# Kernel optimization log

Hardware: AMD Instinct MI355X
Metric: run time of the kernel (lower is better)

## Reference

```python
import jax, jax.numpy as jnp
import numpy as np

N = 50000   # residue nodes
E = 800000  # edges per edge type
T = 3       # edge types
L = 3       # conv layers (len(hidden_channels)-1)
IN, H, ENC, OUT, K = 64, 128, 100, 32, 128
COMMIT = 0.25
EPS = 1e-5


def gelu(x):
    return jax.nn.gelu(x, approximate=False)  # torch nn.GELU default (erf)


def setup_inputs() -> dict:
    key = jax.random.key(0)
    ks = iter(jax.random.split(key, 40))
    p = lambda shp, s=0.05: jax.random.normal(next(ks), shp, jnp.float32) * s
    inp = {
        'x_res': p((N, IN), 1.0),
        'x_AA': p((N, 20), 1.0),
        'edge_index': jax.random.randint(next(ks), (T, 2, E), 0, N, jnp.int32),
        # input block
        'ln_gamma': jnp.ones((IN,), jnp.float32),
        'ln_beta': jnp.zeros((IN,), jnp.float32),
        'W1': p((IN, 2 * H)), 'b1': jnp.zeros((2 * H,), jnp.float32),
        'W2': p((2 * H, H)), 'b2': jnp.zeros((H,), jnp.float32),
        # body: SAGE convs, [layer, edge_type, ...]
        'sage_Wl': p((L, T, H, H)),  # applied to aggregated neighbors
        'sage_Wr': p((L, T, H, H)),  # applied to root
        'sage_b': jnp.zeros((L, T, H), jnp.float32),
        # GraphNorm per layer
        'gn_weight': jnp.ones((L, H), jnp.float32),
        'gn_bias': jnp.zeros((L, H), jnp.float32),
        'gn_scale': jnp.ones((L, H), jnp.float32),  # mean_scale
        # head
        'Wh1': p((H * L, ENC)), 'bh1': jnp.zeros((ENC,), jnp.float32),
        'Wh2': p((ENC, ENC)), 'bh2': jnp.zeros((ENC,), jnp.float32),
        'Wo1': p((ENC + 20, ENC)), 'bo1': jnp.zeros((ENC,), jnp.float32),
        'Wo2': p((ENC, ENC)), 'bo2': jnp.zeros((ENC,), jnp.float32),
        'Wo3': p((ENC, OUT)), 'bo3': jnp.zeros((OUT,), jnp.float32),
        # VQ codebook
        'codebook': p((K, OUT), 0.5),
    }
    return inp


def _sage(x, src, dst, Wl, Wr, b):
    # SAGEConv, mean aggregation: out = Wl @ mean_{src->dst}(x[src]) + Wr @ x + b
    msg = x[src]                                             # [E, H] gather
    s = jax.ops.segment_sum(msg, dst, num_segments=N)        # [N, H] scatter-add
    cnt = jax.ops.segment_sum(jnp.ones((msg.shape[0],), x.dtype), dst, num_segments=N)
    agg = s / jnp.maximum(cnt, 1.0)[:, None]
    return agg @ Wl + x @ Wr + b


def _graphnorm(x, weight, bias, scale):
    # PyG GraphNorm over a single graph
    out = x - scale * x.mean(0)
    var = (out * out).mean(0)
    return out * jax.lax.rsqrt(var + EPS) * weight + bias


def reference(x_res, x_AA, edge_index, ln_gamma, ln_beta, W1, b1, W2, b2,
              sage_Wl, sage_Wr, sage_b, gn_weight, gn_bias, gn_scale,
              Wh1, bh1, Wh2, bh2, Wo1, bo1, Wo2, bo2, Wo3, bo3, codebook):
    # input: LayerNorm + (dropout = identity in eval) + inmlp
    mu = x_res.mean(-1, keepdims=True)
    var = x_res.var(-1, keepdims=True)
    xr = (x_res - mu) * jax.lax.rsqrt(var + EPS) * ln_gamma + ln_beta
    x = gelu(gelu(xr @ W1 + b1) @ W2 + b2)                   # [N, H]

    # body: per-edge-type SAGE conv -> stack-mean -> GELU -> GraphNorm; JK cat
    x_save = []
    for i in range(L):
        xs = [_sage(x, edge_index[t, 0], edge_index[t, 1],
                    sage_Wl[i, t], sage_Wr[i, t], sage_b[i, t]) for t in range(T)]
        x = jnp.mean(jnp.stack(xs, 0), 0)
        x = gelu(x)
        x = _graphnorm(x, gn_weight[i], gn_bias[i], gn_scale[i])
        x_save.append(x)
    x = jnp.concatenate(x_save, axis=1)                      # [N, H*L] JumpingKnowledge cat

    # head
    x = gelu(gelu(x @ Wh1 + bh1) @ Wh2 + bh2)
    x = jnp.concatenate([x, x_AA], axis=1)
    x = gelu(x @ Wo1 + bo1)
    x = gelu(x @ Wo2 + bo2)
    x = jnp.tanh(x @ Wo3 + bo3)                              # [N, OUT]

    # VectorQuantizer (straight-through)
    d = (jnp.sum(x * x, 1, keepdims=True)
         - 2.0 * x @ codebook.T
         + jnp.sum(codebook * codebook, 1)[None, :])         # [N, K]
    idx = jnp.argmin(d, axis=1)
    q = codebook[idx]                                        # [N, OUT]
    e_latent = jnp.mean((jax.lax.stop_gradient(q) - x) ** 2)
    q_latent = jnp.mean((q - jax.lax.stop_gradient(x)) ** 2)
    vq_loss = q_latent + COMMIT * e_latent
    z_q = x + jax.lax.stop_gradient(q - x)
    return z_q, vq_loss
```

## Files before the change

kernel.cpp:

```cpp
#include <hip/hip_runtime.h>

#define N_ 50000
#define E_ 800000
#define T_ 3
#define NG_ (T_ * N_)
#define EPS_ 1e-5f

__device__ __forceinline__ float gelu_f(float x) {
    return 0.5f * x * (1.0f + erff(x * 0.70710678118654752440f));
}

__global__ void k_prep(const float* __restrict__ Wl, const float* __restrict__ Wr,
                       const float* __restrict__ b, float* wls, float* wra, float* ba) {
    int i = blockIdx.x * 256 + threadIdx.x;
    const float third = 1.0f / 3.0f;
    if (i < 9 * 128 * 128) wls[i] = Wl[i] * third;
    if (i < 3 * 128 * 128) {
        int l = i >> 14, rem = i & 16383;
        const float* p = Wr + l * 3 * 16384 + rem;
        wra[i] = (p[0] + p[16384] + p[32768]) * third;
    }
    if (i < 3 * 128) {
        int l = i >> 7, c = i & 127;
        const float* p = b + l * 3 * 128 + c;
        ba[i] = (p[0] + p[128] + p[256]) * third;
    }
}

__global__ void k_count(const int* __restrict__ EI, int* cnt) {
    int i = blockIdx.x * 256 + threadIdx.x;
    if (i >= T_ * E_) return;
    int t = i / E_, e = i - t * E_;
    int d = EI[(t * 2 + 1) * E_ + e];
    atomicAdd(&cnt[t * N_ + d], 1);
}

__global__ void k_alloc(const int* __restrict__ cnt, int* __restrict__ cursor,
                        int* __restrict__ rpA, int* __restrict__ rpB, float* __restrict__ inv) {
    int i = blockIdx.x * 256 + threadIdx.x;
    if (i >= NG_) return;
    int c = cnt[i];
    inv[i] = 1.0f / (float)(c > 0 ? c : 1);
    int s = atomicAdd(cursor, c);
    rpA[i] = s;
    rpB[i] = s;
}

__global__ void k_place(const int* __restrict__ EI, int* __restrict__ rpB, int* __restrict__ csr) {
    int i = blockIdx.x * 256 + threadIdx.x;
    if (i >= T_ * E_) return;
    int t = i / E_, e = i - t * E_;
    int s = EI[(t * 2) * E_ + e];
    int d = EI[(t * 2 + 1) * E_ + e];
    int pos = atomicAdd(&rpB[t * N_ + d], 1);
    csr[pos] = s;
}

__global__ __launch_bounds__(256) void k_inmlp(
    const float* __restrict__ xres, const float* __restrict__ gam, const float* __restrict__ bet,
    const float* __restrict__ W1, const float* __restrict__ b1,
    const float* __restrict__ W2, const float* __restrict__ b2, float* __restrict__ x0) {
    __shared__ float xr[32][68];
    __shared__ float h1[32][260];
    int tid = threadIdx.x;
    int base = blockIdx.x * 32;
    for (int i = 0; i < 2; ++i) {
        int f4 = i * 256 + tid;
        int r = f4 >> 4, c4 = f4 & 15;
        float4 v = make_float4(0.f, 0.f, 0.f, 0.f);
        int gr = base + r;
        if (gr < N_) v = *(const float4*)&xres[gr * 64 + c4 * 4];
        *(float4*)&xr[r][c4 * 4] = v;
    }
    __syncthreads();
    if (tid < 32) {
        int r = tid;
        float s = 0.f;
        for (int k = 0; k < 64; ++k) s += xr[r][k];
        float mu = s * (1.0f / 64.0f);
        float v = 0.f;
        for (int k = 0; k < 64; ++k) { float d = xr[r][k] - mu; v += d * d; }
        float rs = rsqrtf(v * (1.0f / 64.0f) + EPS_);
        for (int k = 0; k < 64; ++k)
            xr[r][k] = (xr[r][k] - mu) * rs * gam[k] + bet[k];
    }
    __syncthreads();
    {
        int tx = tid & 63, ty = tid >> 6;
        int c0 = tx * 4, r0 = ty * 8;
        float acc[8][4];
        for (int r = 0; r < 8; ++r)
            for (int j = 0; j < 4; ++j) acc[r][j] = b1[c0 + j];
        for (int k0 = 0; k0 < 64; k0 += 4) {
            float4 a[8], w[4];
            for (int r = 0; r < 8; ++r) a[r] = *(const float4*)&xr[r0 + r][k0];
            for (int kk = 0; kk < 4; ++kk) w[kk] = *(const float4*)&W1[(k0 + kk) * 256 + c0];
            for (int kk = 0; kk < 4; ++kk)
                for (int r = 0; r < 8; ++r) {
                    float as = (&a[r].x)[kk];
                    acc[r][0] = fmaf(as, w[kk].x, acc[r][0]);
                    acc[r][1] = fmaf(as, w[kk].y, acc[r][1]);
                    acc[r][2] = fmaf(as, w[kk].z, acc[r][2]);
                    acc[r][3] = fmaf(as, w[kk].w, acc[r][3]);
                }
        }
        for (int r = 0; r < 8; ++r)
            for (int j = 0; j < 4; ++j) h1[r0 + r][c0 + j] = gelu_f(acc[r][j]);
    }
    __syncthreads();
    {
        int tx = tid & 31, ty = tid >> 5;
        int c0 = tx * 4, r0 = ty * 4;
        float acc[4][4];
        for (int r = 0; r < 4; ++r)
            for (int j = 0; j < 4; ++j) acc[r][j] = b2[c0 + j];
        for (int k0 = 0; k0 < 256; k0 += 4) {
            float4 a[4], w[4];
            for (int r = 0; r < 4; ++r) a[r] = *(const float4*)&h1[r0 + r][k0];
            for (int kk = 0; kk < 4; ++kk) w[kk] = *(const float4*)&W2[(k0 + kk) * 128 + c0];
            for (int kk = 0; kk < 4; ++kk)
                for (int r = 0; r < 4; ++r) {
                    float as = (&a[r].x)[kk];
                    acc[r][0] = fmaf(as, w[kk].x, acc[r][0]);
                    acc[r][1] = fmaf(as, w[kk].y, acc[r][1]);
                    acc[r][2] = fmaf(as, w[kk].z, acc[r][2]);
                    acc[r][3] = fmaf(as, w[kk].w, acc[r][3]);
                }
        }
        for (int r = 0; r < 4; ++r) {
            int gr = base + r0 + r;
            if (gr < N_) {
                float4 v = make_float4(gelu_f(acc[r][0]), gelu_f(acc[r][1]),
                                       gelu_f(acc[r][2]), gelu_f(acc[r][3]));
                *(float4*)&x0[(long)gr * 128 + c0] = v;
            }
        }
    }
}

__global__ __launch_bounds__(256) void k_gather(
    const int* __restrict__ rpA, const int* __restrict__ cnt, const int* __restrict__ csr,
    const float* __restrict__ inv, const float* __restrict__ X, int ldx, float* __restrict__ agg) {
    int tid = threadIdx.x;
    int g = blockIdx.x * 4 + (tid >> 6);
    if (g >= NG_) return;
    int lane = tid & 63;
    int half = lane >> 5;
    int f = (lane & 31) * 4;
    int start = rpA[g];
    int end = start + cnt[g];
    float4 s = make_float4(0.f, 0.f, 0.f, 0.f);
    for (int e = start + half; e < end; e += 2) {
        int sn = csr[e];
        const float4 v = *(const float4*)&X[(long)sn * ldx + f];
        s.x += v.x; s.y += v.y; s.z += v.z; s.w += v.w;
    }
    s.x += __shfl_xor(s.x, 32);
    s.y += __shfl_xor(s.y, 32);
    s.z += __shfl_xor(s.z, 32);
    s.w += __shfl_xor(s.w, 32);
    if (half == 0) {
        float iv = inv[g];
        float4 o = make_float4(s.x * iv, s.y * iv, s.z * iv, s.w * iv);
        *(float4*)&agg[(long)g * 128 + f] = o;
    }
}

__global__ __launch_bounds__(256) void k_gemm_body(
    const float* __restrict__ X, int ldx, const float* __restrict__ agg,
    const float* __restrict__ wls_l, const float* __restrict__ wra_l, const float* __restrict__ ba_l,
    float* __restrict__ g_out, float* __restrict__ cs_l) {
    __shared__ float xs[64][132];
    __shared__ float sd[8][128];
    int tid = threadIdx.x;
    int base = blockIdx.x * 64;
    int tx = tid & 31, ty = tid >> 5;
    int c0 = tx * 4, r0 = ty * 8;
    float acc[8][4];
    for (int r = 0; r < 8; ++r)
        for (int j = 0; j < 4; ++j) acc[r][j] = ba_l[c0 + j];
    for (int seg = 0; seg < 4; ++seg) {
        const float* src; long ld;
        if (seg < 3) { src = agg + ((long)seg * N_ + base) * 128; ld = 128; }
        else         { src = X + (long)base * ldx; ld = ldx; }
        __syncthreads();
        for (int i = 0; i < 8; ++i) {
            int f4 = i * 256 + tid;
            int r = f4 >> 5, c4 = f4 & 31;
            float4 v = make_float4(0.f, 0.f, 0.f, 0.f);
            if (base + r < N_) v = *(const float4*)&src[(long)r * ld + c4 * 4];
            *(float4*)&xs[r][c4 * 4] = v;
        }
        __syncthreads();
        const float* W = (seg < 3) ? (wls_l + seg * 16384) : wra_l;
        for (int k0 = 0; k0 < 128; k0 += 4) {
            float4 a[8], w[4];
            for (int r = 0; r < 8; ++r) a[r] = *(const float4*)&xs[r0 + r][k0];
            for (int kk = 0; kk < 4; ++kk) w[kk] = *(const float4*)&W[(k0 + kk) * 128 + c0];
            for (int kk = 0; kk < 4; ++kk)
                for (int r = 0; r < 8; ++r) {
                    float as = (&a[r].x)[kk];
                    acc[r][0] = fmaf(as, w[kk].x, acc[r][0]);
                    acc[r][1] = fmaf(as, w[kk].y, acc[r][1]);
                    acc[r][2] = fmaf(as, w[kk].z, acc[r][2]);
                    acc[r][3] = fmaf(as, w[kk].w, acc[r][3]);
                }
        }
    }
    float csum[4] = {0.f, 0.f, 0.f, 0.f};
    for (int r = 0; r < 8; ++r) {
        int gr = base + r0 + r;
        if (gr < N_) {
            float g0 = gelu_f(acc[r][0]), g1 = gelu_f(acc[r][1]);
            float g2 = gelu_f(acc[r][2]), g3 = gelu_f(acc[r][3]);
            *(float4*)&g_out[(long)gr * 128 + c0] = make_float4(g0, g1, g2, g3);
            csum[0] += g0; csum[1] += g1; csum[2] += g2; csum[3] += g3;
        }
    }
    *(float4*)&sd[ty][c0] = make_float4(csum[0], csum[1], csum[2], csum[3]);
    __syncthreads();
    if (tid < 128) {
        float t = 0.f;
        for (int i = 0; i < 8; ++i) t += sd[i][tid];
        atomicAdd(&cs_l[tid], t);
    }
}

__global__ __launch_bounds__(256) void k_pass2(const float* __restrict__ g,
                                               const float* __restrict__ cs_l,
                                               const float* __restrict__ gsc, float* __restrict__ cq_l) {
    __shared__ float sd[256];
    int tid = threadIdx.x;
    int c = tid & 127, half = tid >> 7;
    int base = blockIdx.x * 128 + half * 64;
    float sm = gsc[c] * (cs_l[c] / 50000.0f);
    float s = 0.f;
    for (int i = 0; i < 64; ++i) {
        int r = base + i;
        if (r < N_) { float o = g[(long)r * 128 + c] - sm; s += o * o; }
    }
    sd[tid] = s;
    __syncthreads();
    if (tid < 128) atomicAdd(&cq_l[c], sd[tid] + sd[tid + 128]);
}
__global__ __launch_bounds__(256) void k_pass3(const float* __restrict__ g,
                                               const float* __restrict__ cs_l, const float* __restrict__ cq_l,
                                               const float* __restrict__ gsc,
                                               const float* __restrict__ gw, const float* __restrict__ gb,
                                               float* __restrict__ xs_l) {
    int tid = threadIdx.x;
    int c = tid & 127, half = tid >> 7;
    int base = blockIdx.x * 128 + half * 64;
    float sm = gsc[c] * (cs_l[c] / 50000.0f);
    float var = cq_l[c] / 50000.0f;
    float mul = rsqrtf(var + EPS_) * gw[c];
    float add = gb[c];
    for (int i = 0; i < 64; ++i) {
        int r = base + i;
        if (r < N_) xs_l[(long)r * 384 + c] = (g[(long)r * 128 + c] - sm) * mul + add;
    }
}

__global__ __launch_bounds__(256) void k_head1(const float* __restrict__ xsave,
    const float* __restrict__ Wh1, const float* __restrict__ bh1,
    const float* __restrict__ Wh2, const float* __restrict__ bh2,
    float* __restrict__ h2out) {
    __shared__ float at[64][68];
    __shared__ float h1b[64][104];
    int tid = threadIdx.x;
    int base = blockIdx.x * 64;
    int tx = tid & 31, ty = tid >> 5;
    int c0 = tx * 4, r0 = ty * 8;
    bool valid = (c0 < 100);
    float acc[8][4];
    for (int r = 0; r < 8; ++r)
        for (int j = 0; j < 4; ++j) acc[r][j] = valid ? bh1[c0 + j] : 0.f;
    for (int kt = 0; kt < 6; ++kt) {
        __syncthreads();
        for (int i = 0; i < 4; ++i) {
            int f4 = i * 256 + tid;
            int r = f4 >> 4, c4 = f4 & 15;
            float4 v = make_float4(0.f, 0.f, 0.f, 0.f);
            int gr = base + r;
            if (gr < N_) v = *(const float4*)&xsave[(long)gr * 384 + kt * 64 + c4 * 4];
            *(float4*)&at[r][c4 * 4] = v;
        }
        __syncthreads();
        if (valid) {
            for (int k0 = 0; k0 < 64; k0 += 4) {
                float4 a[8], w[4];
                for (int r = 0; r < 8; ++r) a[r] = *(const float4*)&at[r0 + r][k0];
                for (int kk = 0; kk < 4; ++kk) w[kk] = *(const float4*)&Wh1[(kt * 64 + k0 + kk) * 100 + c0];
                for (int kk = 0; kk < 4; ++kk)
                    for (int r = 0; r < 8; ++r) {
                        float as = (&a[r].x)[kk];
                        acc[r][0] = fmaf(as, w[kk].x, acc[r][0]);
                        acc[r][1] = fmaf(as, w[kk].y, acc[r][1]);
                        acc[r][2] = fmaf(as, w[kk].z, acc[r][2]);
                        acc[r][3] = fmaf(as, w[kk].w, acc[r][3]);
                    }
            }
        }
    }
    __syncthreads();
    if (valid)
        for (int r = 0; r < 8; ++r)
            for (int j = 0; j < 4; ++j) h1b[r0 + r][c0 + j] = gelu_f(acc[r][j]);
    __syncthreads();
    {
        float acc2[8][4];
        for (int r = 0; r < 8; ++r)
            for (int j = 0; j < 4; ++j) acc2[r][j] = valid ? bh2[c0 + j] : 0.f;
        if (valid) {
            for (int k0 = 0; k0 < 100; k0 += 4) {
                float4 a[8], w[4];
                for (int r = 0; r < 8; ++r) a[r] = *(const float4*)&h1b[r0 + r][k0];
                for (int kk = 0; kk < 4; ++kk) w[kk] = *(const float4*)&Wh2[(k0 + kk) * 100 + c0];
                for (int kk = 0; kk < 4; ++kk)
                    for (int r = 0; r < 8; ++r) {
                        float as = (&a[r].x)[kk];
                        acc2[r][0] = fmaf(as, w[kk].x, acc2[r][0]);
                        acc2[r][1] = fmaf(as, w[kk].y, acc2[r][1]);
                        acc2[r][2] = fmaf(as, w[kk].z, acc2[r][2]);
                        acc2[r][3] = fmaf(as, w[kk].w, acc2[r][3]);
                    }
            }
            for (int r = 0; r < 8; ++r) {
                int gr = base + r0 + r;
                if (gr < N_) {
                    float4 v = make_float4(gelu_f(acc2[r][0]), gelu_f(acc2[r][1]),
                                           gelu_f(acc2[r][2]), gelu_f(acc2[r][3]));
                    *(float4*)&h2out[(long)gr * 100 + c0] = v;
                }
            }
        }
    }
}

__global__ __launch_bounds__(128) void k_head2(const float* __restrict__ h2,
    const float* __restrict__ xAA,
    const float* __restrict__ Wo1, const float* __restrict__ bo1,
    const float* __restrict__ Wo2, const float* __restrict__ bo2,
    const float* __restrict__ Wo3, const float* __restrict__ bo3,
    const float* __restrict__ cb, float* __restrict__ zq, float* __restrict__ loss) {
    __shared__ __align__(16) float smem[13216];
    float* A  = smem;
    float* B  = smem + 3968;
    float* XF = smem + 7296;
    float* CB = smem + 8448;
    float* CC = smem + 13056;
    float* SR = smem + 13184;
    int tid = threadIdx.x;
    int base = blockIdx.x * 32;
    for (int i = 0; i < 8; ++i) {
        int f4 = i * 128 + tid;
        int k = f4 >> 3, j4 = f4 & 7;
        float4 v = *(const float4*)&cb[k * 32 + j4 * 4];
        *(float4*)&CB[k * 36 + j4 * 4] = v;
    }
    for (int i = 0; i < 7; ++i) {
        int f4 = i * 128 + tid;
        if (f4 < 800) {
            int r = f4 / 25, c4 = f4 - r * 25;
            float4 v = make_float4(0.f, 0.f, 0.f, 0.f);
            int gr = base + r;
            if (gr < N_) v = *(const float4*)&h2[(long)gr * 100 + c4 * 4];
            *(float4*)&A[r * 124 + c4 * 4] = v;
        }
    }
    for (int i = 0; i < 2; ++i) {
        int f4 = i * 128 + tid;
        if (f4 < 160) {
            int r = f4 / 5, c4 = f4 - r * 5;
            float4 v = make_float4(0.f, 0.f, 0.f, 0.f);
            int gr = base + r;
            if (gr < N_) v = *(const float4*)&xAA[(long)gr * 20 + c4 * 4];
            *(float4*)&A[r * 124 + 100 + c4 * 4] = v;
        }
    }
    __syncthreads();
    if (tid < 128) {
        float s = 0.f;
        for (int j = 0; j < 32; ++j) { float v = CB[tid * 36 + j]; s += v * v; }
        CC[tid] = s;
    }
    int tx = tid & 31, ty = tid >> 5;
    int c0 = tx * 4, r0 = ty * 8;
    bool valid = (c0 < 100);
    {
        float acc[8][4];
        for (int r = 0; r < 8; ++r)
            for (int j = 0; j < 4; ++j) acc[r][j] = valid ? bo1[c0 + j] : 0.f;
        if (valid) {
            for (int k0 = 0; k0 < 120; k0 += 4) {
                float4 a[8], w[4];
                for (int r = 0; r < 8; ++r) a[r] = *(const float4*)&A[(r0 + r) * 124 + k0];
                for (int kk = 0; kk < 4; ++kk) w[kk] = *(const float4*)&Wo1[(k0 + kk) * 100 + c0];
                for (int kk = 0; kk < 4; ++kk)
                    for (int r = 0; r < 8; ++r) {
                        float as = (&a[r].x)[kk];
                        acc[r][0] = fmaf(as, w[kk].x, acc[r][0]);
                        acc[r][1] = fmaf(as, w[kk].y, acc[r][1]);
                        acc[r][2] = fmaf(as, w[kk].z, acc[r][2]);
                        acc[r][3] = fmaf(as, w[kk].w, acc[r][3]);
                    }
            }
        }
        __syncthreads();
        if (valid)
            for (int r = 0; r < 8; ++r)
                for (int j = 0; j < 4; ++j) B[(r0 + r) * 104 + c0 + j] = gelu_f(acc[r][j]);
    }
    __syncthreads();
    {
        float acc[8][4];
        for (int r = 0; r < 8; ++r)
            for (int j = 0; j < 4; ++j) acc[r][j] = valid ? bo2[c0 + j] : 0.f;
        if (valid) {
            for (int k0 = 0; k0 < 100; k0 += 4) {
                float4 a[8], w[4];
                for (int r = 0; r < 8; ++r) a[r] = *(const float4*)&B[(r0 + r) * 104 + k0];
                for (int kk = 0; kk < 4; ++kk) w[kk] = *(const float4*)&Wo2[(k0 + kk) * 100 + c0];
                for (int kk = 0; kk < 4; ++kk)
                    for (int r = 0; r < 8; ++r) {
                        float as = (&a[r].x)[kk];
                        acc[r][0] = fmaf(as, w[kk].x, acc[r][0]);
                        acc[r][1] = fmaf(as, w[kk].y, acc[r][1]);
                        acc[r][2] = fmaf(as, w[kk].z, acc[r][2]);
                        acc[r][3] = fmaf(as, w[kk].w, acc[r][3]);
                    }
            }
        }
        __syncthreads();
        if (valid)
            for (int r = 0; r < 8; ++r)
                for (int j = 0; j < 4; ++j) A[(r0 + r) * 124 + c0 + j] = gelu_f(acc[r][j]);
    }
    __syncthreads();
    {
        int c0b = (tid & 7) * 4, rg = tid >> 3;
        int r0b = rg * 2;
        float acc[2][4];
        for (int r = 0; r < 2; ++r)
            for (int j = 0; j < 4; ++j) acc[r][j] = bo3[c0b + j];
        for (int k0 = 0; k0 < 100; k0 += 4) {
            float4 a[2], w[4];
            for (int r = 0; r < 2; ++r) a[r] = *(const float4*)&A[(r0b + r) * 124 + k0];
            for (int kk = 0; kk < 4; ++kk) w[kk] = *(const float4*)&Wo3[(k0 + kk) * 32 + c0b];
            for (int kk = 0; kk < 4; ++kk)
                for (int r = 0; r < 2; ++r) {
                    float as = (&a[r].x)[kk];
                    acc[r][0] = fmaf(as, w[kk].x, acc[r][0]);
                    acc[r][1] = fmaf(as, w[kk].y, acc[r][1]);
                    acc[r][2] = fmaf(as, w[kk].z, acc[r][2]);
                    acc[r][3] = fmaf(as, w[kk].w, acc[r][3]);
                }
        }
        for (int r = 0; r < 2; ++r)
            for (int j = 0; j < 4; ++j) XF[(r0b + r) * 36 + c0b + j] = tanhf(acc[r][j]);
    }
    __syncthreads();
    {
        int node = tid >> 2, t4 = tid & 3;
        float4 xv[8];
        for (int j4 = 0; j4 < 8; ++j4) xv[j4] = *(const float4*)&XF[node * 36 + j4 * 4];
        float xx = 0.f;
        for (int j4 = 0; j4 < 8; ++j4)
            xx += xv[j4].x * xv[j4].x + xv[j4].y * xv[j4].y + xv[j4].z * xv[j4].z + xv[j4].w * xv[j4].w;
        float best = 3.4e38f;
        int bidx = 0;
        for (int kk = 0; kk < 32; ++kk) {
            int k = kk * 4 + t4;
            const float* cbr = &CB[k * 36];
            float dot = 0.f;
            for (int j4 = 0; j4 < 8; ++j4) {
                float4 cv = *(const float4*)&cbr[j4 * 4];
                dot += cv.x * xv[j4].x + cv.y * xv[j4].y + cv.z * xv[j4].z + cv.w * xv[j4].w;
            }
            float d = fmaf(-2.0f, dot, xx) + CC[k];
            if (d < best) { best = d; bidx = k; }
        }
        for (int off = 1; off < 4; off <<= 1) {
            float ob = __shfl_xor(best, off);
            int oi = __shfl_xor(bidx, off);
            if (ob < best || (ob == best && oi < bidx)) { best = ob; bidx = oi; }
        }
        int gr = base + node;
        if (t4 == 0) {
            float s = 0.f;
            if (gr < N_) {
                const float* q = &CB[bidx * 36];
                for (int j4 = 0; j4 < 8; ++j4) {
                    float4 qv = *(const float4*)&q[j4 * 4];
                    *(float4*)&zq[(long)gr * 32 + j4 * 4] = qv;
                    float4 xvv = xv[j4];
                    float d0 = qv.x - xvv.x, d1 = qv.y - xvv.y, d2 = qv.z - xvv.z, d3 = qv.w - xvv.w;
                    s += d0 * d0 + d1 * d1 + d2 * d2 + d3 * d3;
                }
            }
            SR[node] = s;
        }
    }
    __syncthreads();
    if (tid == 0) {
        float S = 0.f;
        for (int i = 0; i < 32; ++i) S += SR[i];
        atomicAdd(loss, S);
    }
}

__global__ void k_fin(float* dout, const float* loss) {
    if (threadIdx.x == 0 && blockIdx.x == 0)
        dout[(long)N_ * 32] = 1.25f * (loss[0] / 1600000.0f);
}

extern "C" void kernel_launch(void* const* d_in, const int* in_sizes, int n_in,
                              void* d_out, int out_size, void* d_ws, size_t ws_size,
                              hipStream_t stream) {
    const float* x_res = (const float*)d_in[0];
    const float* x_AA  = (const float*)d_in[1];
    const int*   EI    = (const int*)d_in[2];
    const float* ln_g  = (const float*)d_in[3];
    const float* ln_b  = (const float*)d_in[4];
    const float* W1    = (const float*)d_in[5];
    const float* b1    = (const float*)d_in[6];
    const float* W2    = (const float*)d_in[7];
    const float* b2    = (const float*)d_in[8];
    const float* sWl   = (const float*)d_in[9];
    const float* sWr   = (const float*)d_in[10];
    const float* sb    = (const float*)d_in[11];
    const float* gnw   = (const float*)d_in[12];
    const float* gnb   = (const float*)d_in[13];
    const float* gns   = (const float*)d_in[14];
    const float* Wh1   = (const float*)d_in[15];
    const float* bh1   = (const float*)d_in[16];
    const float* Wh2   = (const float*)d_in[17];
    const float* bh2   = (const float*)d_in[18];
    const float* Wo1   = (const float*)d_in[19];
    const float* bo1   = (const float*)d_in[20];
    const float* Wo2   = (const float*)d_in[21];
    const float* bo2   = (const float*)d_in[22];
    const float* Wo3   = (const float*)d_in[23];
    const float* bo3   = (const float*)d_in[24];
    const float* cbk   = (const float*)d_in[25];
    float* out = (float*)d_out;

    float* ws    = (float*)d_ws;
    float* xsave = ws;
    float* x0    = xsave + (size_t)N_ * 384;
    float* agg   = x0 + (size_t)N_ * 128;
    float* gbuf  = agg + (size_t)3 * N_ * 128;
    float* wls   = gbuf + (size_t)N_ * 128;
    float* wra   = wls + 147456;
    float* ba    = wra + 49152;
    int*   cnti  = (int*)(ba + 384);
    int*   cursor= cnti + NG_;
    float* loss  = (float*)(cursor + 1);
    float* cs    = loss + 1;
    float* cq    = cs + 384;
    float* inv   = cq + 384;
    int*   rpA   = (int*)(inv + NG_);
    int*   rpB   = rpA + NG_;
    int*   csr   = rpB + NG_;
    float* h2    = agg + (size_t)N_ * 128;

    hipMemsetAsync(cnti, 0, (NG_ + 2 + 768) * sizeof(int), stream);

    k_prep<<<576, 256, 0, stream>>>(sWl, sWr, sb, wls, wra, ba);
    k_count<<<(T_ * E_ + 255) / 256, 256, 0, stream>>>(EI, cnti);
    k_alloc<<<(NG_ + 255) / 256, 256, 0, stream>>>(cnti, cursor, rpA, rpB, inv);
    k_place<<<(T_ * E_ + 255) / 256, 256, 0, stream>>>(EI, rpB, csr);
    k_inmlp<<<(N_ + 31) / 32, 256, 0, stream>>>(x_res, ln_g, ln_b, W1, b1, W2, b2, x0);

    for (int l = 0; l < 3; ++l) {
        const float* X = (l == 0) ? x0 : (xsave + (size_t)(l - 1) * 128);
        int ldx = (l == 0) ? 128 : 384;
        k_gather<<<NG_ / 4, 256, 0, stream>>>(rpA, cnti, csr, inv, X, ldx, agg);
        k_gemm_body<<<(N_ + 63) / 64, 256, 0, stream>>>(X, ldx, agg,
            wls + (size_t)l * 3 * 16384, wra + (size_t)l * 16384, ba + l * 128,
            gbuf, cs + l * 128);
        k_pass2<<<(N_ + 127) / 128, 256, 0, stream>>>(gbuf, cs + l * 128, gns + l * 128, cq + l * 128);
        k_pass3<<<(N_ + 127) / 128, 256, 0, stream>>>(gbuf, cs + l * 128, cq + l * 128,
                                                      gns + l * 128, gnw + l * 128, gnb + l * 128,
                                                      xsave + (size_t)l * 128);
    }
    k_head1<<<(N_ + 63) / 64, 256, 0, stream>>>(xsave, Wh1, bh1, Wh2, bh2, h2);
    k_head2<<<(N_ + 31) / 32, 128, 0, stream>>>(h2, x_AA, Wo1, bo1, Wo2, bo2, Wo3, bo3,
                                                cbk, out, loss);
    k_fin<<<1, 64, 0, stream>>>(out, loss);
}
```

Measured before the change: 1.659 ms.

## Build CSR via linked lists with warp-scan compaction; widen gather per lane

```diff
diff --git a/kernel.cpp b/kernel.cpp
--- a/kernel.cpp
+++ b/kernel.cpp
@@ -27,33 +27,50 @@
     }
 }
 
-__global__ void k_count(const int* __restrict__ EI, int* cnt) {
+__global__ void k_link(const int* __restrict__ EI, int* __restrict__ head, int* __restrict__ nxt) {
     int i = blockIdx.x * 256 + threadIdx.x;
     if (i >= T_ * E_) return;
     int t = i / E_, e = i - t * E_;
     int d = EI[(t * 2 + 1) * E_ + e];
-    atomicAdd(&cnt[t * N_ + d], 1);
-}
-
-__global__ void k_alloc(const int* __restrict__ cnt, int* __restrict__ cursor,
-                        int* __restrict__ rpA, int* __restrict__ rpB, float* __restrict__ inv) {
-    int i = blockIdx.x * 256 + threadIdx.x;
-    if (i >= NG_) return;
-    int c = cnt[i];
-    inv[i] = 1.0f / (float)(c > 0 ? c : 1);
-    int s = atomicAdd(cursor, c);
-    rpA[i] = s;
-    rpB[i] = s;
-}
-
-__global__ void k_place(const int* __restrict__ EI, int* __restrict__ rpB, int* __restrict__ csr) {
-    int i = blockIdx.x * 256 + threadIdx.x;
-    if (i >= T_ * E_) return;
-    int t = i / E_, e = i - t * E_;
-    int s = EI[(t * 2) * E_ + e];
-    int d = EI[(t * 2 + 1) * E_ + e];
-    int pos = atomicAdd(&rpB[t * N_ + d], 1);
-    csr[pos] = s;
+    nxt[i] = atomicExch(&head[t * N_ + d], i);
+}
+
+__global__ __launch_bounds__(256) void k_compact(
+    const int* __restrict__ EI, const int* __restrict__ head, const int* __restrict__ nxt,
+    int* __restrict__ cursor, int* __restrict__ cnt, int* __restrict__ rpA,
+    float* __restrict__ inv, int* __restrict__ csr) {
+    int tid = threadIdx.x;
+    int g = blockIdx.x * 256 + tid;
+    bool ok = (g < NG_);
+    int lane = tid & 63;
+    int c = 0;
+    int h = -1;
+    if (ok) {
+        h = head[g];
+        int e = h;
+        while (e >= 0) { c++; e = nxt[e]; }
+        cnt[g] = c;
+        inv[g] = 1.0f / (float)(c > 0 ? c : 1);
+    }
+    int x = c;
+    for (int off = 1; off < 64; off <<= 1) {
+        int y = __shfl_up(x, off);
+        if (lane >= off) x += y;
+    }
+    int total = __shfl(x, 63);
+    int base = 0;
+    if (lane == 63 && total > 0) base = atomicAdd(cursor, total);
+    base = __shfl(base, 63);
+    if (ok) {
+        int pos = base + x - c;
+        rpA[g] = pos;
+        int e = h;
+        while (e >= 0) {
+            int t = e / E_, idx = e - t * E_;
+            csr[pos++] = EI[(t * 2) * E_ + idx];
+            e = nxt[e];
+        }
+    }
 }
 
 __global__ __launch_bounds__(256) void k_inmlp(
@@ -145,24 +162,33 @@
     int g = blockIdx.x * 4 + (tid >> 6);
     if (g >= NG_) return;
     int lane = tid & 63;
-    int half = lane >> 5;
-    int f = (lane & 31) * 4;
+    int sub = lane >> 4;
+    int f = (lane & 15) * 8;
     int start = rpA[g];
     int end = start + cnt[g];
-    float4 s = make_float4(0.f, 0.f, 0.f, 0.f);
-    for (int e = start + half; e < end; e += 2) {
+    float4 s0 = make_float4(0.f, 0.f, 0.f, 0.f);
+    float4 s1 = make_float4(0.f, 0.f, 0.f, 0.f);
+    for (int e = start + sub; e < end; e += 4) {
         int sn = csr[e];
-        const float4 v = *(const float4*)&X[(long)sn * ldx + f];
-        s.x += v.x; s.y += v.y; s.z += v.z; s.w += v.w;
-    }
-    s.x += __shfl_xor(s.x, 32);
-    s.y += __shfl_xor(s.y, 32);
-    s.z += __shfl_xor(s.z, 32);
-    s.w += __shfl_xor(s.w, 32);
-    if (half == 0) {
+        const float* row = &X[(long)sn * ldx + f];
+        const float4 v0 = *(const float4*)row;
+        const float4 v1 = *(const float4*)(row + 4);
+        s0.x += v0.x; s0.y += v0.y; s0.z += v0.z; s0.w += v0.w;
+        s1.x += v1.x; s1.y += v1.y; s1.z += v1.z; s1.w += v1.w;
+    }
+    s0.x += __shfl_xor(s0.x, 16); s0.y += __shfl_xor(s0.y, 16);
+    s0.z += __shfl_xor(s0.z, 16); s0.w += __shfl_xor(s0.w, 16);
+    s1.x += __shfl_xor(s1.x, 16); s1.y += __shfl_xor(s1.y, 16);
+    s1.z += __shfl_xor(s1.z, 16); s1.w += __shfl_xor(s1.w, 16);
+    s0.x += __shfl_xor(s0.x, 32); s0.y += __shfl_xor(s0.y, 32);
+    s0.z += __shfl_xor(s0.z, 32); s0.w += __shfl_xor(s0.w, 32);
+    s1.x += __shfl_xor(s1.x, 32); s1.y += __shfl_xor(s1.y, 32);
+    s1.z += __shfl_xor(s1.z, 32); s1.w += __shfl_xor(s1.w, 32);
+    if (sub == 0) {
         float iv = inv[g];
-        float4 o = make_float4(s.x * iv, s.y * iv, s.z * iv, s.w * iv);
-        *(float4*)&agg[(long)g * 128 + f] = o;
+        float* op = &agg[(long)g * 128 + f];
+        *(float4*)op = make_float4(s0.x * iv, s0.y * iv, s0.z * iv, s0.w * iv);
+        *(float4*)(op + 4) = make_float4(s1.x * iv, s1.y * iv, s1.z * iv, s1.w * iv);
     }
 }
 
@@ -553,29 +579,30 @@
     float* wls   = gbuf + (size_t)N_ * 128;
     float* wra   = wls + 147456;
     float* ba    = wra + 49152;
-    int*   cnti  = (int*)(ba + 384);
-    int*   cursor= cnti + NG_;
+    int*   cursor = (int*)(ba + 384);
     float* loss  = (float*)(cursor + 1);
     float* cs    = loss + 1;
     float* cq    = cs + 384;
-    float* inv   = cq + 384;
-    int*   rpA   = (int*)(inv + NG_);
-    int*   rpB   = rpA + NG_;
-    int*   csr   = rpB + NG_;
+    int*   head  = (int*)(cq + 384);
+    int*   nxt   = head + NG_;
+    int*   cnt   = nxt + (size_t)T_ * E_;
+    int*   rpA   = cnt + NG_;
+    float* inv   = (float*)(rpA + NG_);
+    int*   csr   = (int*)(inv + NG_);
     float* h2    = agg + (size_t)N_ * 128;
 
-    hipMemsetAsync(cnti, 0, (NG_ + 2 + 768) * sizeof(int), stream);
+    hipMemsetAsync(cursor, 0, 770 * sizeof(int), stream);
+    hipMemsetAsync(head, 0xFF, NG_ * sizeof(int), stream);
 
     k_prep<<<576, 256, 0, stream>>>(sWl, sWr, sb, wls, wra, ba);
-    k_count<<<(T_ * E_ + 255) / 256, 256, 0, stream>>>(EI, cnti);
-    k_alloc<<<(NG_ + 255) / 256, 256, 0, stream>>>(cnti, cursor, rpA, rpB, inv);
-    k_place<<<(T_ * E_ + 255) / 256, 256, 0, stream>>>(EI, rpB, csr);
+    k_link<<<(T_ * E_ + 255) / 256, 256, 0, stream>>>(EI, head, nxt);
+    k_compact<<<(NG_ + 255) / 256, 256, 0, stream>>>(EI, head, nxt, cursor, cnt, rpA, inv, csr);
     k_inmlp<<<(N_ + 31) / 32, 256, 0, stream>>>(x_res, ln_g, ln_b, W1, b1, W2, b2, x0);
 
     for (int l = 0; l < 3; ++l) {
         const float* X = (l == 0) ? x0 : (xsave + (size_t)(l - 1) * 128);
         int ldx = (l == 0) ? 128 : 384;
-        k_gather<<<NG_ / 4, 256, 0, stream>>>(rpA, cnti, csr, inv, X, ldx, agg);
+        k_gather<<<NG_ / 4, 256, 0, stream>>>(rpA, cnt, csr, inv, X, ldx, agg);
         k_gemm_body<<<(N_ + 63) / 64, 256, 0, stream>>>(X, ldx, agg,
             wls + (size_t)l * 3 * 16384, wra + (size_t)l * 16384, ba + l * 128,
             gbuf, cs + l * 128);
```

Measured after the change: 1.549 ms. 1.07x faster.
